# Kernel optimization log

Measured on AMD Instinct MI355X. Metric: run time of the kernel, lower is better.

Reference implementation:

```python
import jax, jax.numpy as jnp
import numpy as np

EPS = 1e-5

def setup_inputs() -> dict:
    key = jax.random.key(0)
    k1, k2, k3 = jax.random.split(key, 3)
    B, T, F = 64, 512, 1024
    x = jax.random.normal(k1, (B, T, F), dtype=jnp.float32)
    # Linear(width_time, width_time): torch stores weight as (out, in)
    W = jax.random.normal(k2, (T, T), dtype=jnp.float32) * (1.0 / np.sqrt(T))
    b = jax.random.normal(k3, (T,), dtype=jnp.float32) * 0.01
    gamma = jnp.ones((1,), dtype=jnp.float32)
    beta = jnp.zeros((1,), dtype=jnp.float32)
    return {"x": x, "W": W, "b": b, "gamma": gamma, "beta": beta}


def reference(x, W, b, gamma, beta):
    # TSBatchNorm2d: BatchNorm2d(num_features=1) over x.unsqueeze(1)
    # -> stats over all (B, T, F) elements, scalar affine (training-mode batch stats).
    mean = jnp.mean(x)
    var = jnp.var(x)
    y = (x - mean) * jax.lax.rsqrt(var + EPS) * gamma[0] + beta[0]
    # transpose (B,T,F) -> (B,F,T), Linear over time dim, ReLU
    # (dropout is identity in eval mode), transpose back, residual add.
    yt = jnp.swapaxes(y, 1, 2)                      # (B, F, T)
    h = jnp.einsum('bft,ut->bfu', yt, W) + b        # Linear: y @ W.T + b
    h = jax.nn.relu(h)
    return x + jnp.swapaxes(h, 1, 2)                # (B, T, F)
```

## Files before the change

kernel.cpp:

```cpp
#include <hip/hip_runtime.h>
#include <stdint.h>

#define TDIM 512
#define FDIM 1024
#define NTOT 33554432.0f
#define EPS  1e-5f

typedef unsigned short ushort_t;
typedef unsigned short ushort4_t __attribute__((ext_vector_type(4)));
typedef short short8 __attribute__((ext_vector_type(8)));
typedef float floatx4 __attribute__((ext_vector_type(4)));

__device__ __forceinline__ ushort_t f2bf(float f) {
    union { float f; uint32_t u; } v; v.f = f;
    uint32_t r = (v.u + 0x7fffu + ((v.u >> 16) & 1u)) >> 16;
    return (ushort_t)r;
}

__device__ __forceinline__ void async16(const ushort_t* g, ushort_t* l) {
    __builtin_amdgcn_global_load_lds(
        (const __attribute__((address_space(1))) void*)g,
        (__attribute__((address_space(3))) void*)l, 16, 0, 0);
}


__global__ __launch_bounds__(256) void k_stats_transpose(
    const float* __restrict__ x, ushort_t* __restrict__ xTC,
    float2* __restrict__ partials)
{
    __shared__ ushort_t tile[64 * 128];
    __shared__ float red[8];

    int tid = threadIdx.x, bid = blockIdx.x;
    int b  = bid >> 6;
    int t0 = ((bid >> 3) & 7) << 6;
    int ft = bid & 7;
    int f0 = ft << 7;

    int r8 = tid >> 5, c8 = tid & 31;
    const float* xb = x + ((size_t)(b * TDIM + t0) * FDIM) + f0;

    float4 v[8];
#pragma unroll
    for (int p = 0; p < 8; ++p)
        v[p] = *(const float4*)(xb + (size_t)(p * 8 + r8) * FDIM + c8 * 4);

    float s = 0.f, q = 0.f;
#pragma unroll
    for (int p = 0; p < 8; ++p) {
        float4 t = v[p];
        s += t.x + t.y + t.z + t.w;
        q += t.x * t.x + t.y * t.y + t.z * t.z + t.w * t.w;
        ushort4_t pk;
        pk[0] = f2bf(t.x); pk[1] = f2bf(t.y); pk[2] = f2bf(t.z); pk[3] = f2bf(t.w);
        *(ushort4_t*)&tile[(p * 8 + r8) * 128 + c8 * 4] = pk;
    }

#pragma unroll
    for (int off = 32; off > 0; off >>= 1) {
        s += __shfl_down(s, off, 64);
        q += __shfl_down(q, off, 64);
    }
    int lane = tid & 63, w = tid >> 6;
    if (lane == 0) { red[w] = s; red[4 + w] = q; }
    __syncthreads();
    if (tid == 0) {
        partials[bid] = make_float2(red[0] + red[1] + red[2] + red[3],
                                    red[4] + red[5] + red[6] + red[7]);
    }

    int fl = tid & 127, hf = tid >> 7;
    size_t base = ((size_t)((b * 8 + ft) * 16) + (t0 >> 5) + hf) * 4096;
#pragma unroll
    for (int qq = 0; qq < 4; ++qq) {
        int tr = hf * 32 + qq * 8;
        uint32_t w0 = (uint32_t)tile[(tr + 0) * 128 + fl] | ((uint32_t)tile[(tr + 1) * 128 + fl] << 16);
        uint32_t w1 = (uint32_t)tile[(tr + 2) * 128 + fl] | ((uint32_t)tile[(tr + 3) * 128 + fl] << 16);
        uint32_t w2 = (uint32_t)tile[(tr + 4) * 128 + fl] | ((uint32_t)tile[(tr + 5) * 128 + fl] << 16);
        uint32_t w3 = (uint32_t)tile[(tr + 6) * 128 + fl] | ((uint32_t)tile[(tr + 7) * 128 + fl] << 16);
        uint4 o = make_uint4(w0, w1, w2, w3);
        *(uint4*)&xTC[base + (size_t)(qq * 128 + fl) * 8] = o;
    }
}

__global__ __launch_bounds__(256) void k_wcast(
    const float* __restrict__ W, ushort_t* __restrict__ WbC,
    float* __restrict__ rowsumW)
{
    __shared__ float red[4];
    int u = blockIdx.x, tid = threadIdx.x;
    float2 lv = *(const float2*)(W + (size_t)u * 512 + 2 * tid);

    int mt = u >> 7, m = u & 127;
    int kt = tid >> 4;
    int qq = (tid & 15) >> 2;
    int e  = 2 * (tid & 3);
    size_t off = ((size_t)(mt * 16 + kt)) * 4096 + (size_t)(qq * 128 + m) * 8 + e;
    uint32_t pk = (uint32_t)f2bf(lv.x) | ((uint32_t)f2bf(lv.y) << 16);
    *(uint32_t*)&WbC[off] = pk;

    float s = lv.x + lv.y;
#pragma unroll
    for (int off2 = 32; off2 > 0; off2 >>= 1) s += __shfl_down(s, off2, 64);
    int lane = tid & 63, w = tid >> 6;
    if (lane == 0) red[w] = s;
    __syncthreads();
    if (tid == 0) rowsumW[u] = red[0] + red[1] + red[2] + red[3];
}

__global__ __launch_bounds__(256) void k_reduce(
    const float2* __restrict__ partials, const float* __restrict__ rowsumW,
    const float* __restrict__ bias, const float* __restrict__ gamma,
    const float* __restrict__ beta, float* __restrict__ stats,
    float* __restrict__ d)
{
    __shared__ float red[8];
    __shared__ float sac[2];
    int tid = threadIdx.x;
    float s = 0.f, q = 0.f;
#pragma unroll
    for (int i = 0; i < 16; ++i) {
        float2 p = partials[i * 256 + tid];
        s += p.x; q += p.y;
    }
#pragma unroll
    for (int off = 32; off > 0; off >>= 1) {
        s += __shfl_down(s, off, 64);
        q += __shfl_down(q, off, 64);
    }
    int lane = tid & 63, w = tid >> 6;
    if (lane == 0) { red[w] = s; red[4 + w] = q; }
    __syncthreads();
    if (tid == 0) {
        float S = red[0] + red[1] + red[2] + red[3];
        float Q = red[4] + red[5] + red[6] + red[7];
        float mean = S * (1.f / NTOT);
        float var  = Q * (1.f / NTOT) - mean * mean;
        float a    = gamma[0] * rsqrtf(var + EPS);
        float c    = beta[0] - mean * a;
        stats[0] = a;
        sac[0] = a; sac[1] = c;
    }
    __syncthreads();
    float c = sac[1];
    d[tid]       = c * rowsumW[tid]       + bias[tid];
    d[tid + 256] = c * rowsumW[tid + 256] + bias[tid + 256];
}

__global__ __launch_bounds__(256) void k_gemm(
    const ushort_t* __restrict__ WbC, const ushort_t* __restrict__ xTC,
    const float* __restrict__ x, const float* __restrict__ d,
    const float* __restrict__ stats, float* __restrict__ out)
{
    __shared__ ulong smem_raw[2176];
    ushort_t* ldsA = (ushort_t*)smem_raw;
    ushort_t* ldsB = ldsA + 4096;
    float*    ldsC = (float*)smem_raw;

    int tid = threadIdx.x;
    int w = tid >> 6, lane = tid & 63;
    int mt = blockIdx.x;
    int nt = blockIdx.y;
    int b = nt >> 3, ft = nt & 7;
    int wr = w >> 1, wc = w & 1;
    int l15 = lane & 15, q = lane >> 4;

    const ushort_t* Abase = WbC + (size_t)mt * 16 * 4096;
    const ushort_t* Bbase = xTC + (size_t)(b * 8 + ft) * 16 * 4096;

    floatx4 acc[4][4] = {};

    for (int kt = 0; kt < 16; ++kt) {
        const ushort_t* Ag = Abase + kt * 4096 + tid * 8;
        const ushort_t* Bg = Bbase + kt * 4096 + tid * 8;
        async16(Ag,        &ldsA[tid * 8]);
        async16(Ag + 2048, &ldsA[2048 + tid * 8]);
        async16(Bg,        &ldsB[tid * 8]);
        async16(Bg + 2048, &ldsB[2048 + tid * 8]);
        __syncthreads();

        short8 af[4], bfr[4];
#pragma unroll
        for (int i = 0; i < 4; ++i) {
            int m = wr * 64 + i * 16 + l15;
            af[i] = *(const short8*)&ldsA[(q * 128 + m) * 8];
        }
#pragma unroll
        for (int j = 0; j < 4; ++j) {
            int n = wc * 64 + j * 16 + l15;
            bfr[j] = *(const short8*)&ldsB[(q * 128 + n) * 8];
        }
#pragma unroll
        for (int i = 0; i < 4; ++i)
#pragma unroll
            for (int j = 0; j < 4; ++j)
                acc[i][j] = __builtin_amdgcn_mfma_f32_16x16x32_bf16(
                    af[i], bfr[j], acc[i][j], 0, 0, 0);
        __syncthreads();
    }

    float a = stats[0];
    int row = tid >> 3, cs = (tid & 7) * 16;
#pragma unroll
    for (int p = 0; p < 4; ++p) {
        if (wr == (p >> 1)) {
#pragma unroll
            for (int ii = 0; ii < 2; ++ii) {
                int i = (p & 1) * 2 + ii;
                int rl0 = i * 16 + q * 4 - (p & 1) * 32;
#pragma unroll
                for (int j = 0; j < 4; ++j) {
                    int col = wc * 64 + j * 16 + l15;
#pragma unroll
                    for (int r = 0; r < 4; ++r)
                        ldsC[(rl0 + r) * 132 + col] = acc[i][j][r];
                }
            }
        }
        __syncthreads();
        int tg = mt * 128 + p * 32 + row;
        float dt = d[tg];
        size_t gbase = ((size_t)b * TDIM + tg) * FDIM + ft * 128 + cs;
        const float* xr = x + gbase;
        float* orow = out + gbase;
#pragma unroll
        for (int k4 = 0; k4 < 4; ++k4) {
            float4 xv = *(const float4*)(xr + k4 * 4);
            float4 cv = *(const float4*)&ldsC[row * 132 + cs + k4 * 4];
            float4 o;
            o.x = xv.x + fmaxf(a * cv.x + dt, 0.f);
            o.y = xv.y + fmaxf(a * cv.y + dt, 0.f);
            o.z = xv.z + fmaxf(a * cv.z + dt, 0.f);
            o.w = xv.w + fmaxf(a * cv.w + dt, 0.f);
            *(float4*)(orow + k4 * 4) = o;
        }
        __syncthreads();
    }
}

extern "C" void kernel_launch(void* const* d_in, const int* in_sizes, int n_in,
                              void* d_out, int out_size, void* d_ws, size_t ws_size,
                              hipStream_t stream) {
    const float* x     = (const float*)d_in[0];
    const float* W     = (const float*)d_in[1];
    const float* bias  = (const float*)d_in[2];
    const float* gamma = (const float*)d_in[3];
    const float* beta  = (const float*)d_in[4];
    float* out = (float*)d_out;

    char* ws = (char*)d_ws;
    float*    stats    = (float*)ws;
    float*    dvec     = (float*)(ws + 1024);
    float*    rowsumW  = (float*)(ws + 4096);
    float2*   partials = (float2*)(ws + 8192);
    ushort_t* WbC      = (ushort_t*)(ws + (64 << 10));
    ushort_t* xTC      = (ushort_t*)(ws + (1 << 20));

    k_stats_transpose<<<4096, 256, 0, stream>>>(x, xTC, partials);
    k_wcast<<<512, 256, 0, stream>>>(W, WbC, rowsumW);
    k_reduce<<<1, 256, 0, stream>>>(partials, rowsumW, bias, gamma, beta, stats, dvec);
    k_gemm<<<dim3(4, 512), 256, 0, stream>>>(WbC, xTC, x, dvec, stats, out);
}
```

Measured before the change: 326.8 us.

## Double-buffer LDS tiles in GEMM to overlap global loads with MFMA

Doubles the shared-memory staging area into two A/B buffers and prefetches the next k-tile with async global-to-LDS loads while the current tile feeds the MFMAs. This targets the load latency that was exposed every iteration, when the loop waited for its own loads before computing. LDS use per block grows to 32 KB, which may lower occupancy. The loop also relies on the single barrier at the end of each iteration to make the async prefetch visible, with no explicit vmcnt wait, so correctness depends on the barrier draining those loads.

```diff
diff --git a/kernel.cpp b/kernel.cpp
--- a/kernel.cpp
+++ b/kernel.cpp
@@ -152,9 +152,8 @@
     const float* __restrict__ x, const float* __restrict__ d,
     const float* __restrict__ stats, float* __restrict__ out)
 {
-    __shared__ ulong smem_raw[2176];
-    ushort_t* ldsA = (ushort_t*)smem_raw;
-    ushort_t* ldsB = ldsA + 4096;
+    __shared__ ulong smem_raw[4096];
+    ushort_t* lds  = (ushort_t*)smem_raw;
     float*    ldsC = (float*)smem_raw;
 
     int tid = threadIdx.x;
@@ -165,30 +164,41 @@
     int wr = w >> 1, wc = w & 1;
     int l15 = lane & 15, q = lane >> 4;
 
-    const ushort_t* Abase = WbC + (size_t)mt * 16 * 4096;
-    const ushort_t* Bbase = xTC + (size_t)(b * 8 + ft) * 16 * 4096;
+    const ushort_t* Abase = WbC + (size_t)mt * 16 * 4096 + tid * 8;
+    const ushort_t* Bbase = xTC + (size_t)(b * 8 + ft) * 16 * 4096 + tid * 8;
 
     floatx4 acc[4][4] = {};
 
+    async16(Abase,        &lds[tid * 8]);
+    async16(Abase + 2048, &lds[2048 + tid * 8]);
+    async16(Bbase,        &lds[4096 + tid * 8]);
+    async16(Bbase + 2048, &lds[4096 + 2048 + tid * 8]);
+    __syncthreads();
+
     for (int kt = 0; kt < 16; ++kt) {
-        const ushort_t* Ag = Abase + kt * 4096 + tid * 8;
-        const ushort_t* Bg = Bbase + kt * 4096 + tid * 8;
-        async16(Ag,        &ldsA[tid * 8]);
-        async16(Ag + 2048, &ldsA[2048 + tid * 8]);
-        async16(Bg,        &ldsB[tid * 8]);
-        async16(Bg + 2048, &ldsB[2048 + tid * 8]);
-        __syncthreads();
-
+        int cur = (kt & 1) << 13;
+        int nxt = 8192 - cur;
+        if (kt < 15) {
+            const ushort_t* Ag = Abase + (kt + 1) * 4096;
+            const ushort_t* Bg = Bbase + (kt + 1) * 4096;
+            async16(Ag,        &lds[nxt + tid * 8]);
+            async16(Ag + 2048, &lds[nxt + 2048 + tid * 8]);
+            async16(Bg,        &lds[nxt + 4096 + tid * 8]);
+            async16(Bg + 2048, &lds[nxt + 4096 + 2048 + tid * 8]);
+        }
+
+        ushort_t* cA = lds + cur;
+        ushort_t* cB = cA + 4096;
         short8 af[4], bfr[4];
 #pragma unroll
         for (int i = 0; i < 4; ++i) {
             int m = wr * 64 + i * 16 + l15;
-            af[i] = *(const short8*)&ldsA[(q * 128 + m) * 8];
+            af[i] = *(const short8*)&cA[(q * 128 + m) * 8];
         }
 #pragma unroll
         for (int j = 0; j < 4; ++j) {
             int n = wc * 64 + j * 16 + l15;
-            bfr[j] = *(const short8*)&ldsB[(q * 128 + n) * 8];
+            bfr[j] = *(const short8*)&cB[(q * 128 + n) * 8];
         }
 #pragma unroll
         for (int i = 0; i < 4; ++i)
@@ -196,6 +206,7 @@
             for (int j = 0; j < 4; ++j)
                 acc[i][j] = __builtin_amdgcn_mfma_f32_16x16x32_bf16(
                     af[i], bfr[j], acc[i][j], 0, 0, 0);
+
         __syncthreads();
     }
 
```

Result: no change. 323.8 us (-0.9%).

## Double-buffer B tiles in LDS, load A directly from global, XCD-aware block mapping

Applied to the files above, without the earlier changes.

The GEMM kernel now double-buffers only the B (activation) tile in LDS, prefetching the next k-slice while computing on the current one. The A (weight) fragments are read straight from global memory (they are small and cache-resident), which removes half the LDS traffic. The grid is flattened to 1D and block indices are remapped so the four M-tiles sharing a B tile land on the same XCD for L2 reuse. This risks higher global-load latency for A with no LDS staging.

```diff
diff --git a/kernel.cpp b/kernel.cpp
--- a/kernel.cpp
+++ b/kernel.cpp
@@ -153,42 +153,51 @@
     const float* __restrict__ stats, float* __restrict__ out)
 {
     __shared__ ulong smem_raw[2176];
-    ushort_t* ldsA = (ushort_t*)smem_raw;
-    ushort_t* ldsB = ldsA + 4096;
+    ushort_t* lds  = (ushort_t*)smem_raw;
     float*    ldsC = (float*)smem_raw;
 
     int tid = threadIdx.x;
     int w = tid >> 6, lane = tid & 63;
-    int mt = blockIdx.x;
-    int nt = blockIdx.y;
+
+    int hb   = blockIdx.x;
+    int xcd  = hb & 7;
+    int rr   = hb >> 3;
+    int mt   = rr & 3;
+    int nt   = ((rr >> 2) << 3) + xcd;
     int b = nt >> 3, ft = nt & 7;
+
     int wr = w >> 1, wc = w & 1;
     int l15 = lane & 15, q = lane >> 4;
 
     const ushort_t* Abase = WbC + (size_t)mt * 16 * 4096;
-    const ushort_t* Bbase = xTC + (size_t)(b * 8 + ft) * 16 * 4096;
+    const ushort_t* Bbase = xTC + (size_t)(b * 8 + ft) * 16 * 4096 + tid * 8;
+
+    int aoff = (q * 128 + wr * 64 + l15) * 8;
 
     floatx4 acc[4][4] = {};
 
+    async16(Bbase,        &lds[tid * 8]);
+    async16(Bbase + 2048, &lds[2048 + tid * 8]);
+    __syncthreads();
+
     for (int kt = 0; kt < 16; ++kt) {
-        const ushort_t* Ag = Abase + kt * 4096 + tid * 8;
-        const ushort_t* Bg = Bbase + kt * 4096 + tid * 8;
-        async16(Ag,        &ldsA[tid * 8]);
-        async16(Ag + 2048, &ldsA[2048 + tid * 8]);
-        async16(Bg,        &ldsB[tid * 8]);
-        async16(Bg + 2048, &ldsB[2048 + tid * 8]);
-        __syncthreads();
-
+        int cur = (kt & 1) << 12;
+        int nxt = 4096 - cur;
+        if (kt < 15) {
+            const ushort_t* Bg = Bbase + (kt + 1) * 4096;
+            async16(Bg,        &lds[nxt + tid * 8]);
+            async16(Bg + 2048, &lds[nxt + 2048 + tid * 8]);
+        }
+
+        const ushort_t* Ag = Abase + kt * 4096 + aoff;
         short8 af[4], bfr[4];
 #pragma unroll
-        for (int i = 0; i < 4; ++i) {
-            int m = wr * 64 + i * 16 + l15;
-            af[i] = *(const short8*)&ldsA[(q * 128 + m) * 8];
-        }
+        for (int i = 0; i < 4; ++i)
+            af[i] = *(const short8*)&Ag[i * 128];
 #pragma unroll
         for (int j = 0; j < 4; ++j) {
             int n = wc * 64 + j * 16 + l15;
-            bfr[j] = *(const short8*)&ldsB[(q * 128 + n) * 8];
+            bfr[j] = *(const short8*)&lds[cur + (q * 128 + n) * 8];
         }
 #pragma unroll
         for (int i = 0; i < 4; ++i)
@@ -196,6 +205,7 @@
             for (int j = 0; j < 4; ++j)
                 acc[i][j] = __builtin_amdgcn_mfma_f32_16x16x32_bf16(
                     af[i], bfr[j], acc[i][j], 0, 0, 0);
+
         __syncthreads();
     }
 
@@ -259,5 +269,5 @@
     k_stats_transpose<<<4096, 256, 0, stream>>>(x, xTC, partials);
     k_wcast<<<512, 256, 0, stream>>>(W, WbC, rowsumW);
     k_reduce<<<1, 256, 0, stream>>>(partials, rowsumW, bias, gamma, beta, stats, dvec);
-    k_gemm<<<dim3(4, 512), 256, 0, stream>>>(WbC, xTC, x, dvec, stats, out);
-}
+    k_gemm<<<2048, 256, 0, stream>>>(WbC, xTC, x, dvec, stats, out);
+}
```

Measured after the change: 344.5 us. 1.05x slower.
